# Kernel tuning notes

Measured on AMD Instinct MI355X. Metric: run time of the kernel, lower is better.

Reference implementation:

```python
import jax, jax.numpy as jnp
import numpy as np

B, S, HID, HEADS = 8, 1024, 1024, 16
DK = HID // HEADS


def setup_inputs() -> dict:
    key = jax.random.key(0)
    ks = jax.random.split(key, 6)
    scale = 1.0 / np.sqrt(HID)
    return {
        "q": jax.random.normal(ks[0], (B, S, HID), jnp.float32),
        "k": jax.random.normal(ks[1], (B, S, HID), jnp.float32),
        "v": jax.random.normal(ks[2], (B, S, HID), jnp.float32),
        "Wq": jax.random.normal(ks[3], (HID, HID), jnp.float32) * scale,
        "Wk": jax.random.normal(ks[4], (HID, HID), jnp.float32) * scale,
        "Wv": jax.random.normal(ks[5], (HID, HID), jnp.float32) * scale,
        "mask": 1,
    }


def _split_heads(x):
    # [B, S, HID] -> [B, HEADS, S, DK]
    b, s, _ = x.shape
    return x.reshape(b, s, HEADS, DK).transpose(0, 2, 1, 3)


def reference(q, k, v, Wq, Wk, Wv, mask):
    # torch nn.Linear: y = x @ W.T (no bias)
    qh = _split_heads(q @ Wq.T)
    kh = _split_heads(k @ Wk.T)
    vh = _split_heads(v @ Wv.T)

    scores = jnp.einsum("bhqd,bhkd->bhqk", qh, kh) / jnp.sqrt(jnp.asarray(DK, qh.dtype))
    scores = jax.nn.softmax(scores, axis=-1)
    if mask:
        # original zeroes entries where row > col AFTER softmax (keeps upper triangle)
        tri = jnp.triu(jnp.ones((S, S), scores.dtype))
        scores = scores * tri
        # original then transposes the (masked) score matrix before applying to V
        scores = scores.transpose(0, 1, 3, 2)
    out = jnp.einsum("bhqk,bhkd->bhqd", scores, vh)
    # [B, HEADS, S, DK] -> [B, S, HID]
    return out.transpose(0, 2, 1, 3).reshape(q.shape[0], -1, HID)
```

## Files before the change

### kernel.cpp

```cpp
#include <hip/hip_runtime.h>
#include <math.h>

#define B 8
#define S 1024
#define HID 1024
#define HEADS 16
#define DK 64

typedef unsigned short u16;
typedef unsigned int u32;
typedef _Float16 f16;
typedef __attribute__((ext_vector_type(8))) _Float16 half8;
typedef __attribute__((ext_vector_type(4))) _Float16 half4;
typedef __attribute__((ext_vector_type(2))) _Float16 half2;
typedef __attribute__((ext_vector_type(2))) __fp16 fp16x2;
typedef __attribute__((ext_vector_type(4))) float f32x4;

#define GLL16(G, L)                                                         \
    __builtin_amdgcn_global_load_lds(                                       \
        (const __attribute__((address_space(1))) u32*)(G),                  \
        (__attribute__((address_space(3))) u32*)(L), 16, 0, 0)

__device__ __forceinline__ float exp_s(float c) {
#if __has_builtin(__builtin_amdgcn_exp2f)
    return __builtin_amdgcn_exp2f(c * 0.18033688f);
#else
    return __expf(c * 0.125f);
#endif
}

__global__ __launch_bounds__(256) void cast_fused(const float* __restrict__ x,
                                                  const float* __restrict__ w,
                                                  f16* __restrict__ xo,
                                                  f16* __restrict__ wo) {
    const size_t NX = (size_t)B * S * HID / 8;
    const size_t NW = (size_t)HID * HID / 8;
    size_t i = (size_t)blockIdx.x * 256 + threadIdx.x;
    const float* src;
    f16* dst;
    if (i < NX) { src = x + i * 8; dst = xo + i * 8; }
    else if (i < NX + NW) { src = w + (i - NX) * 8; dst = wo + (i - NX) * 8; }
    else return;
    f32x4 a = *(const f32x4*)src;
    f32x4 b = *(const f32x4*)(src + 4);
    half8 h;
    h[0] = (f16)a[0]; h[1] = (f16)a[1]; h[2] = (f16)a[2]; h[3] = (f16)a[3];
    h[4] = (f16)b[0]; h[5] = (f16)b[1]; h[6] = (f16)b[2]; h[7] = (f16)b[3];
    *(half8*)dst = h;
}

template <bool VT>
__global__ __launch_bounds__(256) void proj_mfma(const f16* __restrict__ X,
                                                 const f16* __restrict__ W,
                                                 f16* __restrict__ Y) {
    __shared__ u16 As[128 * 32];
    __shared__ u16 Bs[128 * 32];
    const int tid = threadIdx.x;
    const int wv = tid >> 6, ln = tid & 63;
    const int lr = ln & 15, quad = ln >> 4;
    const int wm = wv >> 1, wn = wv & 1;
    const int row0 = blockIdx.y * 128, col0 = blockIdx.x * 128;

    const int srow = tid >> 2;
    const int sch = tid & 3;

    f32x4 acc[4][4];
    #pragma unroll
    for (int i = 0; i < 4; ++i)
        #pragma unroll
        for (int j = 0; j < 4; ++j) acc[i][j] = (f32x4){0.f, 0.f, 0.f, 0.f};

    for (int k0 = 0; k0 < HID; k0 += 32) {
        #pragma unroll
        for (int p = 0; p < 2; ++p) {
            int r = p * 64 + srow;
            int csw = sch ^ ((r >> 1) & 3);
            GLL16(X + (size_t)(row0 + r) * HID + k0 + csw * 8, As + p * 2048 + tid * 8);
            GLL16(W + (size_t)(col0 + r) * HID + k0 + csw * 8, Bs + p * 2048 + tid * 8);
        }
        __syncthreads();
        half8 a[4], b[4];
        #pragma unroll
        for (int mi = 0; mi < 4; ++mi) {
            int r = wm * 64 + mi * 16 + lr;
            a[mi] = *(const half8*)(As + r * 32 + ((quad ^ ((r >> 1) & 3)) * 8));
        }
        #pragma unroll
        for (int ni = 0; ni < 4; ++ni) {
            int r = wn * 64 + ni * 16 + lr;
            b[ni] = *(const half8*)(Bs + r * 32 + ((quad ^ ((r >> 1) & 3)) * 8));
        }
        #pragma unroll
        for (int mi = 0; mi < 4; ++mi)
            #pragma unroll
            for (int ni = 0; ni < 4; ++ni)
                acc[mi][ni] = __builtin_amdgcn_mfma_f32_16x16x32_f16(
                    a[mi], b[ni], acc[mi][ni], 0, 0, 0);
        __syncthreads();
    }

    if (!VT) {
        #pragma unroll
        for (int mi = 0; mi < 4; ++mi) {
            int m = row0 + wm * 64 + mi * 16 + quad * 4;
            #pragma unroll
            for (int ni = 0; ni < 4; ++ni) {
                int n = col0 + wn * 64 + ni * 16 + lr;
                #pragma unroll
                for (int r = 0; r < 4; ++r)
                    Y[(size_t)(m + r) * HID + n] = (f16)acc[mi][ni][r];
            }
        }
    } else {
        #pragma unroll
        for (int mi = 0; mi < 4; ++mi) {
            int m = row0 + wm * 64 + mi * 16 + quad * 4;
            int bb = m >> 10, s = m & 1023;
            #pragma unroll
            for (int ni = 0; ni < 4; ++ni) {
                int n = col0 + wn * 64 + ni * 16 + lr;
                half4 h4;
                #pragma unroll
                for (int r = 0; r < 4; ++r) h4[r] = (f16)acc[mi][ni][r];
                *(half4*)(Y + ((size_t)(bb * 16 + (n >> 6)) * 64 + (n & 63)) * S + s) = h4;
            }
        }
    }
}

__global__ __launch_bounds__(256) void stats_mfma(const f16* __restrict__ Q,
                                                  const f16* __restrict__ K,
                                                  f16* __restrict__ Vt) {
    const int bh = blockIdx.x, jt = blockIdx.y;
    const int b = bh >> 4, h = bh & 15;
    const int tid = threadIdx.x;
    const int wv = tid >> 6, ln = tid & 63;
    const int lr = ln & 15, quad = ln >> 4;
    __shared__ u16 Qs[256 * 64];
    __shared__ u16 Ks[64 * 64];
    __shared__ float rlL[256];

    #pragma unroll
    for (int p = 0; p < 8; ++p) {
        int r = p * 32 + (tid >> 3);
        int csw = (tid & 7) ^ (r & 7);
        GLL16(Q + (size_t)(b * S + jt * 256 + r) * HID + h * 64 + csw * 8,
              Qs + p * 2048 + tid * 8);
    }
    __syncthreads();
    half8 aq[4][2];
    #pragma unroll
    for (int jsub = 0; jsub < 4; ++jsub) {
        int j = wv * 64 + jsub * 16 + lr;
        #pragma unroll
        for (int kf = 0; kf < 2; ++kf)
            aq[jsub][kf] = *(const half8*)(Qs + j * 64 + (((kf * 4 + quad) ^ (j & 7)) * 8));
    }

    float sl[4][4] = {};

    for (int i0 = 0; i0 < S; i0 += 64) {
        __syncthreads();
        #pragma unroll
        for (int p = 0; p < 2; ++p) {
            int r = p * 32 + (tid >> 3);
            int csw = (tid & 7) ^ (r & 7);
            GLL16(K + (size_t)(b * S + i0 + r) * HID + h * 64 + csw * 8,
                  Ks + p * 2048 + tid * 8);
        }
        __syncthreads();
        #pragma unroll
        for (int isub = 0; isub < 4; ++isub) {
            int il = isub * 16 + lr;
            half8 bk0 = *(const half8*)(Ks + il * 64 + (((0 + quad) ^ (il & 7)) * 8));
            half8 bk1 = *(const half8*)(Ks + il * 64 + (((4 + quad) ^ (il & 7)) * 8));
            #pragma unroll
            for (int jsub = 0; jsub < 4; ++jsub) {
                f32x4 c = {0.f, 0.f, 0.f, 0.f};
                c = __builtin_amdgcn_mfma_f32_16x16x32_f16(aq[jsub][0], bk0, c, 0, 0, 0);
                c = __builtin_amdgcn_mfma_f32_16x16x32_f16(aq[jsub][1], bk1, c, 0, 0, 0);
                #pragma unroll
                for (int r = 0; r < 4; ++r) sl[jsub][r] += exp_s(c[r]);
            }
        }
    }

    #pragma unroll
    for (int jsub = 0; jsub < 4; ++jsub)
        #pragma unroll
        for (int r = 0; r < 4; ++r) {
            float v = sl[jsub][r];
            v += __shfl_xor(v, 1, 64);
            v += __shfl_xor(v, 2, 64);
            v += __shfl_xor(v, 4, 64);
            v += __shfl_xor(v, 8, 64);
            if (lr == 0)
                rlL[wv * 64 + jsub * 16 + quad * 4 + r] = 1.0f / v;
        }
    __syncthreads();

    {
        const int d = tid >> 2, cg = (tid & 3) * 64;
        f16* vrow = Vt + (size_t)(bh * 64 + d) * S + jt * 256 + cg;
        #pragma unroll
        for (int c8 = 0; c8 < 8; ++c8) {
            half8 hv = *(half8*)(vrow + c8 * 8);
            #pragma unroll
            for (int e = 0; e < 8; ++e)
                hv[e] = (f16)((float)hv[e] * rlL[cg + c8 * 8 + e]);
            *(half8*)(vrow + c8 * 8) = hv;
        }
    }
}

__global__ __launch_bounds__(256) void apply_mfma(const f16* __restrict__ Q,
                                                  const f16* __restrict__ K,
                                                  const f16* __restrict__ Vt,
                                                  float* __restrict__ out) {
    const int bh = blockIdx.x;
    const int it2 = (gridDim.y - 1) - blockIdx.y;
    const int b = bh >> 4, h = bh & 15;
    const int tid = threadIdx.x;
    const int wv = tid >> 6, ln = tid & 63;
    const int lr = ln & 15, quad = ln >> 4;
    const int i0b = it2 * 128;
    const int i0w = i0b + wv * 32;

    __shared__ u16 Qs[64 * 64];
    __shared__ u16 Vts[64 * 64];

    half8 bk[2][2];
    #pragma unroll
    for (int isub = 0; isub < 2; ++isub) {
        int i = i0w + isub * 16 + lr;
        #pragma unroll
        for (int kf = 0; kf < 2; ++kf)
            bk[isub][kf] = *(const half8*)(K + (size_t)(b * S + i) * HID + h * 64 +
                                           kf * 32 + quad * 8);
    }

    f32x4 acc[4][2];
    #pragma unroll
    for (int nt = 0; nt < 4; ++nt)
        #pragma unroll
        for (int isub = 0; isub < 2; ++isub) acc[nt][isub] = (f32x4){0.f, 0.f, 0.f, 0.f};

    const int nch = 2 * it2 + 2;
    for (int jc = 0; jc < nch; ++jc) {
        const int j0 = jc * 64;
        __syncthreads();
        #pragma unroll
        for (int p = 0; p < 2; ++p) {
            int r = p * 32 + (tid >> 3);
            int csw = (tid & 7) ^ (r & 7);
            GLL16(Q + (size_t)(b * S + j0 + r) * HID + h * 64 + csw * 8,
                  Qs + p * 2048 + tid * 8);
        }
        #pragma unroll
        for (int p = 0; p < 2; ++p) {
            int d = p * 32 + (tid >> 3);
            int csw = (tid & 7) ^ (d & 7);
            GLL16(Vt + (size_t)(bh * 64 + d) * S + j0 + csw * 8,
                  Vts + p * 2048 + tid * 8);
        }
        __syncthreads();

        #pragma unroll
        for (int jsub = 0; jsub < 4; ++jsub) {
            const int jbase = j0 + jsub * 16;
            if (jbase > i0w + 31) break;

            const int jl = jsub * 16 + lr;
            half8 aq0 = *(const half8*)(Qs + jl * 64 + (((0 + quad) ^ (jl & 7)) * 8));
            half8 aq1 = *(const half8*)(Qs + jl * 64 + (((4 + quad) ^ (jl & 7)) * 8));
            half4 av[4];
            #pragma unroll
            for (int nt = 0; nt < 4; ++nt) {
                int d = nt * 16 + lr;
                int ch = (jsub * 2 + (quad >> 1)) ^ (d & 7);
                av[nt] = *(const half4*)(Vts + d * 64 + ch * 8 + (quad & 1) * 4);
            }

            #pragma unroll
            for (int isub = 0; isub < 2; ++isub) {
                const int ib = i0w + isub * 16;
                if (jbase > ib + 15) continue;
                f32x4 c = {0.f, 0.f, 0.f, 0.f};
                c = __builtin_amdgcn_mfma_f32_16x16x32_f16(aq0, bk[isub][0], c, 0, 0, 0);
                c = __builtin_amdgcn_mfma_f32_16x16x32_f16(aq1, bk[isub][1], c, 0, 0, 0);
                float w0 = exp_s(c[0]), w1 = exp_s(c[1]);
                float w2 = exp_s(c[2]), w3 = exp_s(c[3]);
                if (jbase + 15 > ib) {
                    const int i_col = ib + lr;
                    const int jq = jbase + quad * 4;
                    if (jq + 0 > i_col) w0 = 0.f;
                    if (jq + 1 > i_col) w1 = 0.f;
                    if (jq + 2 > i_col) w2 = 0.f;
                    if (jq + 3 > i_col) w3 = 0.f;
                }
                fp16x2 q0 = __builtin_amdgcn_cvt_pkrtz(w0, w1);
                fp16x2 q1 = __builtin_amdgcn_cvt_pkrtz(w2, w3);
                half2 p0 = __builtin_bit_cast(half2, q0);
                half2 p1 = __builtin_bit_cast(half2, q1);
                half4 bw;
                bw[0] = p0[0]; bw[1] = p0[1]; bw[2] = p1[0]; bw[3] = p1[1];
                #pragma unroll
                for (int nt = 0; nt < 4; ++nt)
                    acc[nt][isub] = __builtin_amdgcn_mfma_f32_16x16x16f16(
                        av[nt], bw, acc[nt][isub], 0, 0, 0);
            }
        }
    }

    #pragma unroll
    for (int isub = 0; isub < 2; ++isub) {
        int i = i0w + isub * 16 + lr;
        #pragma unroll
        for (int nt = 0; nt < 4; ++nt)
            *(f32x4*)(out + (size_t)(b * S + i) * HID + h * 64 + nt * 16 + quad * 4) =
                acc[nt][isub];
    }
}

extern "C" void kernel_launch(void* const* d_in, const int* in_sizes, int n_in,
                              void* d_out, int out_size, void* d_ws, size_t ws_size,
                              hipStream_t stream) {
    const float* q  = (const float*)d_in[0];
    const float* k  = (const float*)d_in[1];
    const float* v  = (const float*)d_in[2];
    const float* Wq = (const float*)d_in[3];
    const float* Wk = (const float*)d_in[4];
    const float* Wv = (const float*)d_in[5];

    const size_t SZ = (size_t)B * S * HID;
    const size_t WZ = (size_t)HID * HID;

    char* p = (char*)d_ws;
    f16* xb = (f16*)p;      p += SZ * 2;
    f16* wb = (f16*)p;      p += WZ * 2;
    f16* Qb = (f16*)p;      p += SZ * 2;
    f16* Kb = (f16*)p;      p += SZ * 2;
    f16* Vt = (f16*)p;      p += SZ * 2;

    float* out = (float*)d_out;

    const int ncast = (int)((SZ + WZ) / 8 + 255) / 256;
    dim3 gproj(HID / 128, (B * S) / 128);

    cast_fused<<<ncast, 256, 0, stream>>>(q, Wq, xb, wb);
    proj_mfma<false><<<gproj, 256, 0, stream>>>(xb, wb, Qb);

    cast_fused<<<ncast, 256, 0, stream>>>(k, Wk, xb, wb);
    proj_mfma<false><<<gproj, 256, 0, stream>>>(xb, wb, Kb);

    cast_fused<<<ncast, 256, 0, stream>>>(v, Wv, xb, wb);
    proj_mfma<true><<<gproj, 256, 0, stream>>>(xb, wb, Vt);

    stats_mfma<<<dim3(B * HEADS, S / 256), 256, 0, stream>>>(Qb, Kb, Vt);
    apply_mfma<<<dim3(B * HEADS, S / 128), 256, 0, stream>>>(Qb, Kb, Vt, out);
}
```

Before: 317.6 us.

## Batch QKV casts and projections into single launches, shrink stats tiles

```diff
diff --git a/kernel.cpp b/kernel.cpp
--- a/kernel.cpp
+++ b/kernel.cpp
@@ -29,18 +29,23 @@
 #endif
 }
 
-__global__ __launch_bounds__(256) void cast_fused(const float* __restrict__ x,
-                                                  const float* __restrict__ w,
-                                                  f16* __restrict__ xo,
-                                                  f16* __restrict__ wo) {
-    const size_t NX = (size_t)B * S * HID / 8;
-    const size_t NW = (size_t)HID * HID / 8;
-    size_t i = (size_t)blockIdx.x * 256 + threadIdx.x;
+__global__ __launch_bounds__(256) void cast_all(
+    const float* __restrict__ q, const float* __restrict__ k,
+    const float* __restrict__ v, const float* __restrict__ Wq,
+    const float* __restrict__ Wk, const float* __restrict__ Wv,
+    f16* __restrict__ oq, f16* __restrict__ ok, f16* __restrict__ ov,
+    f16* __restrict__ owq, f16* __restrict__ owk, f16* __restrict__ owv) {
+    const size_t SZ = (size_t)B * S * HID;
+    const size_t WZ = (size_t)HID * HID;
+    size_t e = ((size_t)blockIdx.x * 256 + threadIdx.x) * 8;
     const float* src;
     f16* dst;
-    if (i < NX) { src = x + i * 8; dst = xo + i * 8; }
-    else if (i < NX + NW) { src = w + (i - NX) * 8; dst = wo + (i - NX) * 8; }
-    else return;
+    if (e < SZ)               { src = q + e;               dst = oq + e; }
+    else if (e < 2 * SZ)      { src = k + (e - SZ);        dst = ok + (e - SZ); }
+    else if (e < 3 * SZ)      { src = v + (e - 2 * SZ);    dst = ov + (e - 2 * SZ); }
+    else if (e < 3 * SZ + WZ) { src = Wq + (e - 3 * SZ);   dst = owq + (e - 3 * SZ); }
+    else if (e < 3 * SZ + 2 * WZ) { src = Wk + (e - 3 * SZ - WZ); dst = owk + (e - 3 * SZ - WZ); }
+    else                      { src = Wv + (e - 3 * SZ - 2 * WZ); dst = owv + (e - 3 * SZ - 2 * WZ); }
     f32x4 a = *(const f32x4*)src;
     f32x4 b = *(const f32x4*)(src + 4);
     half8 h;
@@ -49,17 +54,23 @@
     *(half8*)dst = h;
 }
 
-template <bool VT>
-__global__ __launch_bounds__(256) void proj_mfma(const f16* __restrict__ X,
-                                                 const f16* __restrict__ W,
-                                                 f16* __restrict__ Y) {
+__global__ __launch_bounds__(256) void proj_mfma_b(
+    const f16* __restrict__ Xq, const f16* __restrict__ Xk,
+    const f16* __restrict__ Xv, const f16* __restrict__ Wq,
+    const f16* __restrict__ Wk, const f16* __restrict__ Wv,
+    f16* __restrict__ Qb, f16* __restrict__ Kb, f16* __restrict__ Vt) {
+    const int z = blockIdx.x % 3;
+    const int cx = blockIdx.x / 3;
+    const f16* __restrict__ X = (z == 0) ? Xq : (z == 1) ? Xk : Xv;
+    const f16* __restrict__ W = (z == 0) ? Wq : (z == 1) ? Wk : Wv;
+
     __shared__ u16 As[128 * 32];
     __shared__ u16 Bs[128 * 32];
     const int tid = threadIdx.x;
     const int wv = tid >> 6, ln = tid & 63;
     const int lr = ln & 15, quad = ln >> 4;
     const int wm = wv >> 1, wn = wv & 1;
-    const int row0 = blockIdx.y * 128, col0 = blockIdx.x * 128;
+    const int row0 = blockIdx.y * 128, col0 = cx * 128;
 
     const int srow = tid >> 2;
     const int sch = tid & 3;
@@ -99,7 +110,8 @@
         __syncthreads();
     }
 
-    if (!VT) {
+    if (z < 2) {
+        f16* __restrict__ Y = (z == 0) ? Qb : Kb;
         #pragma unroll
         for (int mi = 0; mi < 4; ++mi) {
             int m = row0 + wm * 64 + mi * 16 + quad * 4;
@@ -122,7 +134,7 @@
                 half4 h4;
                 #pragma unroll
                 for (int r = 0; r < 4; ++r) h4[r] = (f16)acc[mi][ni][r];
-                *(half4*)(Y + ((size_t)(bb * 16 + (n >> 6)) * 64 + (n & 63)) * S + s) = h4;
+                *(half4*)(Vt + ((size_t)(bb * 16 + (n >> 6)) * 64 + (n & 63)) * S + s) = h4;
             }
         }
     }
@@ -136,28 +148,15 @@
     const int tid = threadIdx.x;
     const int wv = tid >> 6, ln = tid & 63;
     const int lr = ln & 15, quad = ln >> 4;
-    __shared__ u16 Qs[256 * 64];
     __shared__ u16 Ks[64 * 64];
-    __shared__ float rlL[256];
-
-    #pragma unroll
-    for (int p = 0; p < 8; ++p) {
-        int r = p * 32 + (tid >> 3);
-        int csw = (tid & 7) ^ (r & 7);
-        GLL16(Q + (size_t)(b * S + jt * 256 + r) * HID + h * 64 + csw * 8,
-              Qs + p * 2048 + tid * 8);
-    }
-    __syncthreads();
-    half8 aq[4][2];
-    #pragma unroll
-    for (int jsub = 0; jsub < 4; ++jsub) {
-        int j = wv * 64 + jsub * 16 + lr;
-        #pragma unroll
-        for (int kf = 0; kf < 2; ++kf)
-            aq[jsub][kf] = *(const half8*)(Qs + j * 64 + (((kf * 4 + quad) ^ (j & 7)) * 8));
-    }
-
-    float sl[4][4] = {};
+    __shared__ float rlL[64];
+
+    const int j = jt * 64 + wv * 16 + lr;
+    const f16* qrow = Q + (size_t)(b * S + j) * HID + h * 64;
+    half8 aq0 = *(const half8*)(qrow + quad * 8);
+    half8 aq1 = *(const half8*)(qrow + 32 + quad * 8);
+
+    float sl[4] = {0.f, 0.f, 0.f, 0.f};
 
     for (int i0 = 0; i0 < S; i0 += 64) {
         __syncthreads();
@@ -174,36 +173,30 @@
             int il = isub * 16 + lr;
             half8 bk0 = *(const half8*)(Ks + il * 64 + (((0 + quad) ^ (il & 7)) * 8));
             half8 bk1 = *(const half8*)(Ks + il * 64 + (((4 + quad) ^ (il & 7)) * 8));
-            #pragma unroll
-            for (int jsub = 0; jsub < 4; ++jsub) {
-                f32x4 c = {0.f, 0.f, 0.f, 0.f};
-                c = __builtin_amdgcn_mfma_f32_16x16x32_f16(aq[jsub][0], bk0, c, 0, 0, 0);
-                c = __builtin_amdgcn_mfma_f32_16x16x32_f16(aq[jsub][1], bk1, c, 0, 0, 0);
-                #pragma unroll
-                for (int r = 0; r < 4; ++r) sl[jsub][r] += exp_s(c[r]);
-            }
-        }
-    }
-
-    #pragma unroll
-    for (int jsub = 0; jsub < 4; ++jsub)
-        #pragma unroll
-        for (int r = 0; r < 4; ++r) {
-            float v = sl[jsub][r];
-            v += __shfl_xor(v, 1, 64);
-            v += __shfl_xor(v, 2, 64);
-            v += __shfl_xor(v, 4, 64);
-            v += __shfl_xor(v, 8, 64);
-            if (lr == 0)
-                rlL[wv * 64 + jsub * 16 + quad * 4 + r] = 1.0f / v;
-        }
+            f32x4 c = {0.f, 0.f, 0.f, 0.f};
+            c = __builtin_amdgcn_mfma_f32_16x16x32_f16(aq0, bk0, c, 0, 0, 0);
+            c = __builtin_amdgcn_mfma_f32_16x16x32_f16(aq1, bk1, c, 0, 0, 0);
+            #pragma unroll
+            for (int r = 0; r < 4; ++r) sl[r] += exp_s(c[r]);
+        }
+    }
+
+    #pragma unroll
+    for (int r = 0; r < 4; ++r) {
+        float v = sl[r];
+        v += __shfl_xor(v, 1, 64);
+        v += __shfl_xor(v, 2, 64);
+        v += __shfl_xor(v, 4, 64);
+        v += __shfl_xor(v, 8, 64);
+        if (lr == 0) rlL[wv * 16 + quad * 4 + r] = 1.0f / v;
+    }
     __syncthreads();
 
     {
-        const int d = tid >> 2, cg = (tid & 3) * 64;
-        f16* vrow = Vt + (size_t)(bh * 64 + d) * S + jt * 256 + cg;
-        #pragma unroll
-        for (int c8 = 0; c8 < 8; ++c8) {
+        const int d = tid >> 2, cg = (tid & 3) * 16;
+        f16* vrow = Vt + (size_t)(bh * 64 + d) * S + jt * 64 + cg;
+        #pragma unroll
+        for (int c8 = 0; c8 < 2; ++c8) {
             half8 hv = *(half8*)(vrow + c8 * 8);
             #pragma unroll
             for (int e = 0; e < 8; ++e)
@@ -335,27 +328,27 @@
     const size_t SZ = (size_t)B * S * HID;
     const size_t WZ = (size_t)HID * HID;
 
+    f16* xq = (f16*)d_out;
+    f16* xk = xq + SZ;
+
     char* p = (char*)d_ws;
-    f16* xb = (f16*)p;      p += SZ * 2;
-    f16* wb = (f16*)p;      p += WZ * 2;
+    f16* xv = (f16*)p;      p += SZ * 2;
+    f16* wq = (f16*)p;      p += WZ * 2;
+    f16* wk = (f16*)p;      p += WZ * 2;
+    f16* wv_ = (f16*)p;     p += WZ * 2;
     f16* Qb = (f16*)p;      p += SZ * 2;
     f16* Kb = (f16*)p;      p += SZ * 2;
     f16* Vt = (f16*)p;      p += SZ * 2;
 
     float* out = (float*)d_out;
 
-    const int ncast = (int)((SZ + WZ) / 8 + 255) / 256;
-    dim3 gproj(HID / 128, (B * S) / 128);
-
-    cast_fused<<<ncast, 256, 0, stream>>>(q, Wq, xb, wb);
-    proj_mfma<false><<<gproj, 256, 0, stream>>>(xb, wb, Qb);
-
-    cast_fused<<<ncast, 256, 0, stream>>>(k, Wk, xb, wb);
-    proj_mfma<false><<<gproj, 256, 0, stream>>>(xb, wb, Kb);
-
-    cast_fused<<<ncast, 256, 0, stream>>>(v, Wv, xb, wb);
-    proj_mfma<true><<<gproj, 256, 0, stream>>>(xb, wb, Vt);
-
-    stats_mfma<<<dim3(B * HEADS, S / 256), 256, 0, stream>>>(Qb, Kb, Vt);
+    const int ncast = (int)((3 * SZ + 3 * WZ) / 8 / 256);
+    cast_all<<<ncast, 256, 0, stream>>>(q, k, v, Wq, Wk, Wv,
+                                        xq, xk, xv, wq, wk, wv_);
+
+    proj_mfma_b<<<dim3(3 * HID / 128, (B * S) / 128), 256, 0, stream>>>(
+        xq, xk, xv, wq, wk, wv_, Qb, Kb, Vt);
+
+    stats_mfma<<<dim3(B * HEADS, S / 64), 256, 0, stream>>>(Qb, Kb, Vt);
     apply_mfma<<<dim3(B * HEADS, S / 128), 256, 0, stream>>>(Qb, Kb, Vt, out);
 }
```

New measurement: 298.3 us. 6.1% less time.
